# Kernel optimization log

Hardware: AMD Instinct MI355X
Metric: run time of the kernel (lower is better)

The kernel has to match this reference:

```python
import jax, jax.numpy as jnp
import numpy as np

G = 256       # number of graphs in batch
NPG = 400     # nodes per graph (hardcoded in module)
DEG = 32      # avg degree
FIN = 400     # input feature dim
H = 64        # hidden_channels
N = G * NPG
E = G * NPG * DEG


def _glorot(key, fan_in, fan_out):
    lim = float(np.sqrt(6.0 / (fan_in + fan_out)))
    return jax.random.uniform(key, (fan_in, fan_out), jnp.float32, -lim, lim)


def setup_inputs() -> dict:
    key = jax.random.key(0)
    ks = jax.random.split(key, 12)
    x = jax.random.normal(ks[0], (N, FIN), jnp.float32)
    # intra-graph random edges, then offset by graph id so edges never cross graphs
    src = jax.random.randint(ks[1], (G, NPG * DEG), 0, NPG)
    dst = jax.random.randint(ks[2], (G, NPG * DEG), 0, NPG)
    offs = (jnp.arange(G) * NPG)[:, None]
    edge_index = jnp.stack([(src + offs).reshape(-1), (dst + offs).reshape(-1)]).astype(jnp.int32)
    edge_weight = jax.random.uniform(ks[3], (E,), jnp.float32)
    return {
        "x": x,
        "edge_index": edge_index,
        "edge_weight": edge_weight,
        "W1": _glorot(ks[4], FIN, H), "b1": jnp.zeros((H,), jnp.float32),
        "W2": _glorot(ks[5], H, H),   "b2": jnp.zeros((H,), jnp.float32),
        "W3": _glorot(ks[6], H, H),   "b3": jnp.zeros((H,), jnp.float32),
        "Wc": _glorot(ks[7], NPG * H, H), "bc": jnp.zeros((H,), jnp.float32),
        "Wl": _glorot(ks[8], H, 2),   "bl": jnp.zeros((2,), jnp.float32),
    }


def _gcn_conv(x, W, b, row, col, norm, n):
    # PyG GCNConv: out[col] += norm * (x @ W)[row]; then + bias
    h = x @ W                                   # [n, out]
    msg = norm[:, None] * h[row]                # [E+n, out] gather + scale
    return jax.ops.segment_sum(msg, col, num_segments=n) + b


def reference(x, edge_index, edge_weight, W1, b1, W2, b2, W3, b3, Wc, bc, Wl, bl):
    n = x.shape[0]
    loop = jnp.arange(n, dtype=edge_index.dtype)
    row = jnp.concatenate([edge_index[0], loop])            # sources (with self-loops)
    col = jnp.concatenate([edge_index[1], loop])            # targets
    ew = jnp.concatenate([edge_weight, jnp.ones((n,), edge_weight.dtype)])
    # symmetric normalization: deg^{-1/2}[row] * w * deg^{-1/2}[col]
    deg = jax.ops.segment_sum(ew, col, num_segments=n)
    dinv = jnp.where(deg > 0, jax.lax.rsqrt(deg), 0.0)
    norm = dinv[row] * ew * dinv[col]

    h = jax.nn.relu(_gcn_conv(x, W1, b1, row, col, norm, n))
    h = jax.nn.relu(_gcn_conv(h, W2, b2, row, col, norm, n))
    h = _gcn_conv(h, W3, b3, row, col, norm, n)
    # per-graph flatten of 400 nodes -> lincomb (vectorized form of the Python loop)
    g = h.reshape(-1, NPG * H) @ Wc + bc        # [G, H]
    # dropout p=0.5 skipped (eval mode)
    return g @ Wl + bl                          # [G, 2]
```

## Files before the change

kernel.cpp:

```cpp
#include <hip/hip_runtime.h>
#include <hip/hip_bf16.h>
#include <stdint.h>

#define G 256
#define NPG 400
#define DEG 32
#define FIN 400
#define H 64
#define NN (G*NPG)
#define EE (G*NPG*DEG)
#define EPG (NPG*DEG)
#define CPG (EPG+NPG)
#define NTILE 25
#define ATS 420
#define HTS 72
#define MTSZ 25600

#define W1F_OFF 0
#define W1F_N   (13*4*64*8)
#define W2F_OFF (W1F_OFF + W1F_N)
#define W2F_N   (2*4*64*8)
#define W3F_OFF (W2F_OFF + W2F_N)
#define WCF_OFF (W3F_OFF + W2F_N)
#define WCF_N   (800*4*64*8)
#define WF_TOT  (WCF_OFF + WCF_N)

#define FB_M1   1792
#define FB_NORM (FB_M1 + G)
#define FB_WC   (FB_NORM + WCF_N/256)

typedef __attribute__((ext_vector_type(8))) _Float16 h8;
typedef __attribute__((ext_vector_type(4))) float f32x4;

static __device__ __forceinline__ unsigned packh2(float a, float b) {
  unsigned short ua = __builtin_bit_cast(unsigned short, (_Float16)a);
  unsigned short ub = __builtin_bit_cast(unsigned short, (_Float16)b);
  return (unsigned)ua | ((unsigned)ub << 16);
}

static __device__ __forceinline__ h8 cvt8(float4 a, float4 b) {
  h8 r;
  r[0] = (_Float16)a.x; r[1] = (_Float16)a.y; r[2] = (_Float16)a.z; r[3] = (_Float16)a.w;
  r[4] = (_Float16)b.x; r[5] = (_Float16)b.y; r[6] = (_Float16)b.z; r[7] = (_Float16)b.w;
  return r;
}

__global__ __launch_bounds__(256) void kPackW(
    const float* __restrict__ W1, const float* __restrict__ W2,
    const float* __restrict__ W3,
    _Float16* __restrict__ wf, float* __restrict__ gbuf)
{
  int idx = blockIdx.x*256 + threadIdx.x;
  if (idx < G*H) gbuf[idx] = 0.f;
  if (idx >= WCF_OFF) return;
  if (idx < W2F_OFF) {
    int i = idx;
    int j = i & 7, ln = (i >> 3) & 63, nt = (i >> 9) & 3, ks = i >> 11;
    int k = ks*32 + (ln >> 4)*8 + j, col = nt*16 + (ln & 15);
    wf[idx] = (k < FIN) ? (_Float16)W1[k*H + col] : (_Float16)0.f;
  } else if (idx < W3F_OFF) {
    int i = idx - W2F_OFF;
    int j = i & 7, ln = (i >> 3) & 63, nt = (i >> 9) & 3, ks = i >> 11;
    wf[idx] = (_Float16)W2[(ks*32 + (ln >> 4)*8 + j)*H + nt*16 + (ln & 15)];
  } else {
    int i = idx - W3F_OFF;
    int j = i & 7, ln = (i >> 3) & 63, nt = (i >> 9) & 3, ks = i >> 11;
    wf[idx] = (_Float16)W3[(ks*32 + (ln >> 4)*8 + j)*H + nt*16 + (ln & 15)];
  }
}

__global__ __launch_bounds__(256) void kFront(
    const float* __restrict__ x, const int* __restrict__ ei,
    const float* __restrict__ ew, const float* __restrict__ Wc,
    const _Float16* __restrict__ wfr, _Float16* __restrict__ wfw,
    uint2* __restrict__ ent, uint32_t* __restrict__ boff,
    _Float16* __restrict__ mt1)
{
  extern __shared__ char smem[];
  const int b = blockIdx.x, tid = threadIdx.x;

  if (b < FB_M1) {
    _Float16* sh = (_Float16*)smem;
    const int lane = tid & 63, wave = tid >> 6;
    const int l15 = lane & 15, kgrp = lane >> 4;
    const int g = b / 7, bt = b % 7;
    const int node_l = bt*64 + wave*16 + l15;
    const int arow = (node_l < NPG) ? node_l : NPG-1;
    const float* xp = x + ((size_t)g*NPG + arow)*FIN;

    h8 af[13];
    #pragma unroll
    for (int ks = 0; ks < 13; ++ks) {
      int kb = ks*32 + kgrp*8;
      if (kb + 8 <= FIN) {
        float4 a0 = *(const float4*)(xp + kb);
        float4 a1 = *(const float4*)(xp + kb + 4);
        af[ks] = cvt8(a0, a1);
      } else {
        h8 z;
        #pragma unroll
        for (int j = 0; j < 8; ++j) z[j] = (_Float16)0.f;
        af[ks] = z;
      }
    }
    f32x4 acc[4] = {{0,0,0,0},{0,0,0,0},{0,0,0,0},{0,0,0,0}};
    for (int nt = 0; nt < 4; ++nt)
      for (int ks = 0; ks < 13; ++ks) {
        h8 bf = *(const h8*)&wfr[W1F_OFF + (((size_t)ks*4 + nt)*64 + lane)*8];
        acc[nt] = __builtin_amdgcn_mfma_f32_16x16x32_f16(af[ks], bf, acc[nt], 0, 0, 0);
      }
    #pragma unroll
    for (int nt = 0; nt < 4; ++nt) {
      int feat = nt*16 + l15;
      #pragma unroll
      for (int r = 0; r < 4; ++r)
        sh[(wave*16 + kgrp*4 + r)*HTS + feat] = (_Float16)acc[nt][r];
    }
    __syncthreads();
    const unsigned short* shu = (const unsigned short*)sh;
    for (int i = tid; i < 64*16; i += 256) {
      int feat = i >> 4, seg = i & 15;
      int nl = seg*4, gn = bt*64 + nl;
      if (gn < NPG) {
        uint2 u;
        u.x = (unsigned)shu[(nl+0)*HTS + feat] | ((unsigned)shu[(nl+1)*HTS + feat] << 16);
        u.y = (unsigned)shu[(nl+2)*HTS + feat] | ((unsigned)shu[(nl+3)*HTS + feat] << 16);
        *(uint2*)&mt1[(size_t)g*MTSZ + feat*400 + gn] = u;
      }
    }
  } else if (b < FB_NORM) {
    float* deg = (float*)smem;
    float* dv  = deg + NPG;
    uint32_t* bcnt = (uint32_t*)(dv + NPG);
    uint32_t* bpos = bcnt + 32;
    const int g = b - FB_M1;
    const int ebase = g*EPG, nbase = g*NPG;
    const int* rowp = ei;
    const int* colp = ei + EE;
    if (tid < NTILE) bcnt[tid] = 0u;
    for (int v = tid; v < NPG; v += 256) deg[v] = 1.0f;
    __syncthreads();
    for (int e = tid; e < EPG; e += 256) {
      int c = colp[ebase+e] - nbase;
      atomicAdd(&deg[c], ew[ebase+e]);
      atomicAdd(&bcnt[c >> 4], 1u);
    }
    __syncthreads();
    for (int v = tid; v < NPG; v += 256) dv[v] = rsqrtf(deg[v]);
    if (tid == 0) {
      uint32_t s = 0;
      #pragma unroll
      for (int t = 0; t < NTILE; ++t) {
        uint32_t c = bcnt[t] + 16u;
        bcnt[t] = s; bpos[t] = s; s += c;
      }
    }
    __syncthreads();
    if (tid < NTILE) boff[g*32 + tid] = bcnt[tid];
    if (tid == NTILE) boff[g*32 + NTILE] = (uint32_t)CPG;
    uint2* eb = ent + (size_t)g*CPG;
    for (int e = tid; e < EPG; e += 256) {
      int src = rowp[ebase+e] - nbase;
      int dst = colp[ebase+e] - nbase;
      float nm = dv[src] * ew[ebase+e] * dv[dst];
      uint32_t p = atomicAdd(&bpos[dst >> 4], 1u);
      eb[p] = make_uint2(((unsigned)dst << 16) | (unsigned)src, __float_as_uint(nm));
    }
    for (int v = tid; v < NPG; v += 256) {
      uint32_t p = atomicAdd(&bpos[v >> 4], 1u);
      eb[p] = make_uint2(((unsigned)v << 16) | (unsigned)v, __float_as_uint(dv[v]*dv[v]));
    }
  } else {
    int idx = (b - FB_NORM)*256 + tid;
    int j = idx & 7, ln = (idx >> 3) & 63, nt = (idx >> 9) & 3, kt = idx >> 11;
    int kp = kt*32 + (ln >> 4)*8 + j;
    int node = kp % 400, feat = kp / 400;
    int col = nt*16 + (ln & 15);
    wfw[WCF_OFF + idx] = (_Float16)Wc[((size_t)node*64 + feat)*64 + col];
  }
}

template<int WMUL>
__global__ __launch_bounds__(256, 4) void kAgg(
    const _Float16* __restrict__ mtin, const _Float16* __restrict__ wfn,
    const float* __restrict__ bias,
    const uint2* __restrict__ ent, const uint32_t* __restrict__ boff,
    _Float16* __restrict__ out)
{
  extern __shared__ char smem[];
  float* sAT = (float*)smem;
  _Float16* sh = (_Float16*)(smem + 16*ATS*4);
  const int tid = threadIdx.x, lane = tid & 63;
  const int l15 = lane & 15, kgrp = lane >> 4;
  const int bid = blockIdx.x;
  const int g = bid & 255, t = bid >> 8;
  const int t0 = t*16;
  const int nt = tid >> 6;
  const uint2* eb = ent + (size_t)g*CPG;
  const uint32_t s0 = boff[g*32 + t], s1 = boff[g*32 + t + 1];

  h8 BF[13];
  const _Float16* mrow = mtin + (size_t)g*MTSZ + (nt*16 + l15)*400;
  #pragma unroll
  for (int ks = 0; ks < 13; ++ks)
    BF[ks] = *(const h8*)(mrow + ks*32 + kgrp*8);
  const float bv = bias[nt*16 + l15];
  h8 WF2[2];
  if (WMUL) {
    WF2[0] = *(const h8*)&wfn[((size_t)(0*4 + nt)*64 + lane)*8];
    WF2[1] = *(const h8*)&wfn[((size_t)(1*4 + nt)*64 + lane)*8];
  }
  const uint32_t e0 = s0 + tid;
  uint2 E0 = make_uint2(0,0), E1 = make_uint2(0,0), E2 = make_uint2(0,0);
  if (e0       < s1) E0 = eb[e0];
  if (e0 + 256 < s1) E1 = eb[e0 + 256];
  if (e0 + 512 < s1) E2 = eb[e0 + 512];

  { float4* p = (float4*)sAT;
    for (int i = tid; i < 16*ATS/4; i += 256) p[i] = make_float4(0,0,0,0); }
  __syncthreads();

  if (e0       < s1) atomicAdd(&sAT[((int)(E0.x >> 16) - t0)*ATS + (int)(E0.x & 0xffffu)], __uint_as_float(E0.y));
  if (e0 + 256 < s1) atomicAdd(&sAT[((int)(E1.x >> 16) - t0)*ATS + (int)(E1.x & 0xffffu)], __uint_as_float(E1.y));
  if (e0 + 512 < s1) atomicAdd(&sAT[((int)(E2.x >> 16) - t0)*ATS + (int)(E2.x & 0xffffu)], __uint_as_float(E2.y));
  for (uint32_t e = e0 + 768; e < s1; e += 256) {
    uint2 E = eb[e];
    atomicAdd(&sAT[((int)(E.x >> 16) - t0)*ATS + (int)(E.x & 0xffffu)], __uint_as_float(E.y));
  }
  __syncthreads();

  f32x4 acc = {0,0,0,0};
  const float* ap = &sAT[l15*ATS];
  #pragma unroll
  for (int ks = 0; ks < 13; ++ks) {
    int kb = ks*32 + kgrp*8;
    float4 a0 = *(const float4*)(ap + kb);
    float4 a1 = *(const float4*)(ap + kb + 4);
    acc = __builtin_amdgcn_mfma_f32_16x16x32_f16(cvt8(a0, a1), BF[ks], acc, 0, 0, 0);
  }

  const int node0 = t0 + kgrp*4;
  if (!WMUL) {
    uint2 u;
    u.x = packh2(acc[0] + bv, acc[1] + bv);
    u.y = packh2(acc[2] + bv, acc[3] + bv);
    *(uint2*)&out[(size_t)g*MTSZ + (nt*16 + l15)*400 + node0] = u;
  } else {
    #pragma unroll
    for (int r = 0; r < 4; ++r)
      sh[(kgrp*4 + r)*HTS + nt*16 + l15] = (_Float16)fmaxf(acc[r] + bv, 0.f);
    __syncthreads();
    f32x4 acc2 = {0,0,0,0};
    const _Float16* hp = &sh[l15*HTS];
    acc2 = __builtin_amdgcn_mfma_f32_16x16x32_f16(*(const h8*)(hp + kgrp*8),      WF2[0], acc2, 0, 0, 0);
    acc2 = __builtin_amdgcn_mfma_f32_16x16x32_f16(*(const h8*)(hp + 32 + kgrp*8), WF2[1], acc2, 0, 0, 0);
    uint2 u;
    u.x = packh2(acc2[0], acc2[1]);
    u.y = packh2(acc2[2], acc2[3]);
    *(uint2*)&out[(size_t)g*MTSZ + (nt*16 + l15)*400 + node0] = u;
  }
}

__global__ __launch_bounds__(256) void kRead(
    const _Float16* __restrict__ h3, const _Float16* __restrict__ wfc,
    float* __restrict__ gbuf)
{
  const int tid = threadIdx.x, lane = tid & 63, nt = tid >> 6;
  const int l15 = lane & 15, kgrp = lane >> 4;
  const int rt = blockIdx.x & 15, kc = blockIdx.x >> 4;
  f32x4 acc = {0,0,0,0};
  const _Float16* hp = h3 + (size_t)(rt*16 + l15)*MTSZ;
  for (int ks = 0; ks < 25; ++ks) {
    int kt = kc*25 + ks;
    h8 af = *(const h8*)(hp + kt*32 + kgrp*8);
    h8 bf = *(const h8*)(wfc + (((size_t)kt*4 + nt)*64 + lane)*8);
    acc = __builtin_amdgcn_mfma_f32_16x16x32_f16(af, bf, acc, 0, 0, 0);
  }
  #pragma unroll
  for (int r = 0; r < 4; ++r)
    atomicAdd(&gbuf[(size_t)(rt*16 + kgrp*4 + r)*H + nt*16 + l15], acc[r]);
}

__global__ __launch_bounds__(64) void k6_final(
    const float* __restrict__ gbuf, const float* __restrict__ bc,
    const float* __restrict__ Wl, const float* __restrict__ bl,
    float* __restrict__ out)
{
  int t = blockIdx.x*64 + threadIdx.x;
  int gr = t >> 1, c = t & 1;
  float acc = bl[c];
  for (int f = 0; f < H; ++f)
    acc += (gbuf[gr*H + f] + bc[f]) * Wl[f*2 + c];
  out[gr*2 + c] = acc;
}

extern "C" void kernel_launch(void* const* d_in, const int* in_sizes, int n_in,
                              void* d_out, int out_size, void* d_ws, size_t ws_size,
                              hipStream_t stream)
{
  const float* x  = (const float*)d_in[0];
  const int*   ei = (const int*)d_in[1];
  const float* ew = (const float*)d_in[2];
  const float* W1 = (const float*)d_in[3];
  const float* b1 = (const float*)d_in[4];
  const float* W2 = (const float*)d_in[5];
  const float* b2 = (const float*)d_in[6];
  const float* W3 = (const float*)d_in[7];
  const float* b3 = (const float*)d_in[8];
  const float* Wc = (const float*)d_in[9];
  const float* bc = (const float*)d_in[10];
  const float* Wl = (const float*)d_in[11];
  const float* bl = (const float*)d_in[12];
  float* out = (float*)d_out;
  (void)ws_size;

  char* ws = (char*)d_ws;
  size_t o = 0;
  uint2*     ent  = (uint2*)(ws + o);     o += (size_t)G*CPG*8;
  uint32_t*  boff = (uint32_t*)(ws + o);  o += (size_t)G*32*4;
  _Float16*  mtA  = (_Float16*)(ws + o);  o += (size_t)G*MTSZ*2 + 256;
  _Float16*  mtB  = (_Float16*)(ws + o);  o += (size_t)G*MTSZ*2 + 256;
  _Float16*  wf   = (_Float16*)(ws + o);  o += (size_t)WF_TOT*2;
  float*     gbuf = (float*)(ws + o);     o += (size_t)G*H*4;

  kPackW<<<(WCF_OFF+255)/256, 256, 0, stream>>>(W1, W2, W3, wf, gbuf);
  kFront<<<FB_WC, 256, 64*HTS*2, stream>>>(x, ei, ew, Wc, wf, wf, ent, boff, mtA);
  const int aggLds = 16*ATS*4 + 16*HTS*2;
  kAgg<1><<<NTILE*G, 256, aggLds, stream>>>(mtA, wf + W2F_OFF, b1, ent, boff, mtB);
  kAgg<1><<<NTILE*G, 256, aggLds, stream>>>(mtB, wf + W3F_OFF, b2, ent, boff, mtA);
  kAgg<0><<<NTILE*G, 256, aggLds, stream>>>(mtA, wf, b3, ent, boff, mtB);
  kRead<<<512, 256, 0, stream>>>(mtB, wf + WCF_OFF, gbuf);
  k6_final<<<8, 64, 0, stream>>>(gbuf, bc, Wl, bl, out);
}
```

Before: 306.6 us.

## Split fused front kernel into separate norm, M1 GEMM, and Wc-pack kernels

```diff
diff --git a/kernel.cpp b/kernel.cpp
--- a/kernel.cpp
+++ b/kernel.cpp
@@ -23,11 +23,6 @@
 #define W3F_OFF (W2F_OFF + W2F_N)
 #define WCF_OFF (W3F_OFF + W2F_N)
 #define WCF_N   (800*4*64*8)
-#define WF_TOT  (WCF_OFF + WCF_N)
-
-#define FB_M1   1792
-#define FB_NORM (FB_M1 + G)
-#define FB_WC   (FB_NORM + WCF_N/256)
 
 typedef __attribute__((ext_vector_type(8))) _Float16 h8;
 typedef __attribute__((ext_vector_type(4))) float f32x4;
@@ -69,114 +64,114 @@
   }
 }
 
-__global__ __launch_bounds__(256) void kFront(
-    const float* __restrict__ x, const int* __restrict__ ei,
-    const float* __restrict__ ew, const float* __restrict__ Wc,
-    const _Float16* __restrict__ wfr, _Float16* __restrict__ wfw,
-    uint2* __restrict__ ent, uint32_t* __restrict__ boff,
+__global__ __launch_bounds__(256) void kWcPack(
+    const float* __restrict__ Wc, _Float16* __restrict__ wf)
+{
+  int idx = blockIdx.x*256 + threadIdx.x;
+  int j = idx & 7, ln = (idx >> 3) & 63, nt = (idx >> 9) & 3, kt = idx >> 11;
+  int kp = kt*32 + (ln >> 4)*8 + j;
+  int node = kp % 400, feat = kp / 400;
+  int col = nt*16 + (ln & 15);
+  wf[WCF_OFF + idx] = (_Float16)Wc[((size_t)node*64 + feat)*64 + col];
+}
+
+__global__ __launch_bounds__(1024) void kNorm(
+    const int* __restrict__ ei, const float* __restrict__ ew,
+    uint2* __restrict__ ent, uint32_t* __restrict__ boff)
+{
+  __shared__ float deg[NPG];
+  __shared__ float dv[NPG];
+  __shared__ uint32_t bcnt[32], bpos[32];
+  const int g = blockIdx.x, tid = threadIdx.x;
+  const int ebase = g*EPG, nbase = g*NPG;
+  const int* rowp = ei;
+  const int* colp = ei + EE;
+  if (tid < NTILE) bcnt[tid] = 0u;
+  for (int v = tid; v < NPG; v += 1024) deg[v] = 1.0f;
+  __syncthreads();
+  for (int e = tid; e < EPG; e += 1024) {
+    int c = colp[ebase+e] - nbase;
+    atomicAdd(&deg[c], ew[ebase+e]);
+    atomicAdd(&bcnt[c >> 4], 1u);
+  }
+  __syncthreads();
+  for (int v = tid; v < NPG; v += 1024) dv[v] = rsqrtf(deg[v]);
+  if (tid == 0) {
+    uint32_t s = 0;
+    #pragma unroll
+    for (int t = 0; t < NTILE; ++t) {
+      uint32_t c = bcnt[t] + 16u;
+      bcnt[t] = s; bpos[t] = s; s += c;
+    }
+  }
+  __syncthreads();
+  if (tid < NTILE) boff[g*32 + tid] = bcnt[tid];
+  if (tid == NTILE) boff[g*32 + NTILE] = (uint32_t)CPG;
+  uint2* eb = ent + (size_t)g*CPG;
+  for (int e = tid; e < EPG; e += 1024) {
+    int src = rowp[ebase+e] - nbase;
+    int dst = colp[ebase+e] - nbase;
+    float nm = dv[src] * ew[ebase+e] * dv[dst];
+    uint32_t p = atomicAdd(&bpos[dst >> 4], 1u);
+    eb[p] = make_uint2(((unsigned)dst << 16) | (unsigned)src, __float_as_uint(nm));
+  }
+  for (int v = tid; v < NPG; v += 1024) {
+    uint32_t p = atomicAdd(&bpos[v >> 4], 1u);
+    eb[p] = make_uint2(((unsigned)v << 16) | (unsigned)v, __float_as_uint(dv[v]*dv[v]));
+  }
+}
+
+__global__ __launch_bounds__(256, 4) void kM1(
+    const float* __restrict__ x, const _Float16* __restrict__ wf,
     _Float16* __restrict__ mt1)
 {
-  extern __shared__ char smem[];
-  const int b = blockIdx.x, tid = threadIdx.x;
-
-  if (b < FB_M1) {
-    _Float16* sh = (_Float16*)smem;
-    const int lane = tid & 63, wave = tid >> 6;
-    const int l15 = lane & 15, kgrp = lane >> 4;
-    const int g = b / 7, bt = b % 7;
-    const int node_l = bt*64 + wave*16 + l15;
-    const int arow = (node_l < NPG) ? node_l : NPG-1;
-    const float* xp = x + ((size_t)g*NPG + arow)*FIN;
-
-    h8 af[13];
+  __shared__ _Float16 sh[64*HTS];
+  const int tid = threadIdx.x, lane = tid & 63, wave = tid >> 6;
+  const int l15 = lane & 15, kgrp = lane >> 4;
+  const int g = blockIdx.y, b = blockIdx.x;
+  const int node_l = b*64 + wave*16 + l15;
+  const int arow = (node_l < NPG) ? node_l : NPG-1;
+  const float* xp = x + ((size_t)g*NPG + arow)*FIN;
+
+  h8 af[13];
+  #pragma unroll
+  for (int ks = 0; ks < 13; ++ks) {
+    int kb = ks*32 + kgrp*8;
+    if (kb + 8 <= FIN) {
+      float4 a0 = *(const float4*)(xp + kb);
+      float4 a1 = *(const float4*)(xp + kb + 4);
+      af[ks] = cvt8(a0, a1);
+    } else {
+      h8 z;
+      #pragma unroll
+      for (int j = 0; j < 8; ++j) z[j] = (_Float16)0.f;
+      af[ks] = z;
+    }
+  }
+  f32x4 acc[4] = {{0,0,0,0},{0,0,0,0},{0,0,0,0},{0,0,0,0}};
+  for (int nt = 0; nt < 4; ++nt)
+    for (int ks = 0; ks < 13; ++ks) {
+      h8 bf = *(const h8*)&wf[W1F_OFF + (((size_t)ks*4 + nt)*64 + lane)*8];
+      acc[nt] = __builtin_amdgcn_mfma_f32_16x16x32_f16(af[ks], bf, acc[nt], 0, 0, 0);
+    }
+  #pragma unroll
+  for (int nt = 0; nt < 4; ++nt) {
+    int feat = nt*16 + l15;
     #pragma unroll
-    for (int ks = 0; ks < 13; ++ks) {
-      int kb = ks*32 + kgrp*8;
-      if (kb + 8 <= FIN) {
-        float4 a0 = *(const float4*)(xp + kb);
-        float4 a1 = *(const float4*)(xp + kb + 4);
-        af[ks] = cvt8(a0, a1);
-      } else {
-        h8 z;
-        #pragma unroll
-        for (int j = 0; j < 8; ++j) z[j] = (_Float16)0.f;
-        af[ks] = z;
-      }
+    for (int r = 0; r < 4; ++r)
+      sh[(wave*16 + kgrp*4 + r)*HTS + feat] = (_Float16)acc[nt][r];
+  }
+  __syncthreads();
+  const unsigned short* shu = (const unsigned short*)sh;
+  for (int i = tid; i < 64*16; i += 256) {
+    int feat = i >> 4, seg = i & 15;
+    int nl = seg*4, gn = b*64 + nl;
+    if (gn < NPG) {
+      uint2 u;
+      u.x = (unsigned)shu[(nl+0)*HTS + feat] | ((unsigned)shu[(nl+1)*HTS + feat] << 16);
+      u.y = (unsigned)shu[(nl+2)*HTS + feat] | ((unsigned)shu[(nl+3)*HTS + feat] << 16);
+      *(uint2*)&mt1[(size_t)g*MTSZ + feat*400 + gn] = u;
     }
-    f32x4 acc[4] = {{0,0,0,0},{0,0,0,0},{0,0,0,0},{0,0,0,0}};
-    for (int nt = 0; nt < 4; ++nt)
-      for (int ks = 0; ks < 13; ++ks) {
-        h8 bf = *(const h8*)&wfr[W1F_OFF + (((size_t)ks*4 + nt)*64 + lane)*8];
-        acc[nt] = __builtin_amdgcn_mfma_f32_16x16x32_f16(af[ks], bf, acc[nt], 0, 0, 0);
-      }
-    #pragma unroll
-    for (int nt = 0; nt < 4; ++nt) {
-      int feat = nt*16 + l15;
-      #pragma unroll
-      for (int r = 0; r < 4; ++r)
-        sh[(wave*16 + kgrp*4 + r)*HTS + feat] = (_Float16)acc[nt][r];
-    }
-    __syncthreads();
-    const unsigned short* shu = (const unsigned short*)sh;
-    for (int i = tid; i < 64*16; i += 256) {
-      int feat = i >> 4, seg = i & 15;
-      int nl = seg*4, gn = bt*64 + nl;
-      if (gn < NPG) {
-        uint2 u;
-        u.x = (unsigned)shu[(nl+0)*HTS + feat] | ((unsigned)shu[(nl+1)*HTS + feat] << 16);
-        u.y = (unsigned)shu[(nl+2)*HTS + feat] | ((unsigned)shu[(nl+3)*HTS + feat] << 16);
-        *(uint2*)&mt1[(size_t)g*MTSZ + feat*400 + gn] = u;
-      }
-    }
-  } else if (b < FB_NORM) {
-    float* deg = (float*)smem;
-    float* dv  = deg + NPG;
-    uint32_t* bcnt = (uint32_t*)(dv + NPG);
-    uint32_t* bpos = bcnt + 32;
-    const int g = b - FB_M1;
-    const int ebase = g*EPG, nbase = g*NPG;
-    const int* rowp = ei;
-    const int* colp = ei + EE;
-    if (tid < NTILE) bcnt[tid] = 0u;
-    for (int v = tid; v < NPG; v += 256) deg[v] = 1.0f;
-    __syncthreads();
-    for (int e = tid; e < EPG; e += 256) {
-      int c = colp[ebase+e] - nbase;
-      atomicAdd(&deg[c], ew[ebase+e]);
-      atomicAdd(&bcnt[c >> 4], 1u);
-    }
-    __syncthreads();
-    for (int v = tid; v < NPG; v += 256) dv[v] = rsqrtf(deg[v]);
-    if (tid == 0) {
-      uint32_t s = 0;
-      #pragma unroll
-      for (int t = 0; t < NTILE; ++t) {
-        uint32_t c = bcnt[t] + 16u;
-        bcnt[t] = s; bpos[t] = s; s += c;
-      }
-    }
-    __syncthreads();
-    if (tid < NTILE) boff[g*32 + tid] = bcnt[tid];
-    if (tid == NTILE) boff[g*32 + NTILE] = (uint32_t)CPG;
-    uint2* eb = ent + (size_t)g*CPG;
-    for (int e = tid; e < EPG; e += 256) {
-      int src = rowp[ebase+e] - nbase;
-      int dst = colp[ebase+e] - nbase;
-      float nm = dv[src] * ew[ebase+e] * dv[dst];
-      uint32_t p = atomicAdd(&bpos[dst >> 4], 1u);
-      eb[p] = make_uint2(((unsigned)dst << 16) | (unsigned)src, __float_as_uint(nm));
-    }
-    for (int v = tid; v < NPG; v += 256) {
-      uint32_t p = atomicAdd(&bpos[v >> 4], 1u);
-      eb[p] = make_uint2(((unsigned)v << 16) | (unsigned)v, __float_as_uint(dv[v]*dv[v]));
-    }
-  } else {
-    int idx = (b - FB_NORM)*256 + tid;
-    int j = idx & 7, ln = (idx >> 3) & 63, nt = (idx >> 9) & 3, kt = idx >> 11;
-    int kp = kt*32 + (ln >> 4)*8 + j;
-    int node = kp % 400, feat = kp / 400;
-    int col = nt*16 + (ln & 15);
-    wfw[WCF_OFF + idx] = (_Float16)Wc[((size_t)node*64 + feat)*64 + col];
   }
 }
 
@@ -320,14 +315,16 @@
   uint32_t*  boff = (uint32_t*)(ws + o);  o += (size_t)G*32*4;
   _Float16*  mtA  = (_Float16*)(ws + o);  o += (size_t)G*MTSZ*2 + 256;
   _Float16*  mtB  = (_Float16*)(ws + o);  o += (size_t)G*MTSZ*2 + 256;
-  _Float16*  wf   = (_Float16*)(ws + o);  o += (size_t)WF_TOT*2;
+  _Float16*  wf   = (_Float16*)(ws + o);  o += (size_t)(WCF_OFF+WCF_N)*2;
   float*     gbuf = (float*)(ws + o);     o += (size_t)G*H*4;
 
   kPackW<<<(WCF_OFF+255)/256, 256, 0, stream>>>(W1, W2, W3, wf, gbuf);
-  kFront<<<FB_WC, 256, 64*HTS*2, stream>>>(x, ei, ew, Wc, wf, wf, ent, boff, mtA);
+  kNorm<<<G, 1024, 0, stream>>>(ei, ew, ent, boff);
+  kM1<<<dim3(7, G), 256, 0, stream>>>(x, wf, mtA);
   const int aggLds = 16*ATS*4 + 16*HTS*2;
   kAgg<1><<<NTILE*G, 256, aggLds, stream>>>(mtA, wf + W2F_OFF, b1, ent, boff, mtB);
   kAgg<1><<<NTILE*G, 256, aggLds, stream>>>(mtB, wf + W3F_OFF, b2, ent, boff, mtA);
+  kWcPack<<<WCF_N/256, 256, 0, stream>>>(Wc, wf);
   kAgg<0><<<NTILE*G, 256, aggLds, stream>>>(mtA, wf, b3, ent, boff, mtB);
   kRead<<<512, 256, 0, stream>>>(mtB, wf + WCF_OFF, gbuf);
   k6_final<<<8, 64, 0, stream>>>(gbuf, bc, Wl, bl, out);
```

After: 271.6 us. 1.13x faster.
